# Kernel tuning notes

Hardware: AMD Instinct MI355X
Metric: run time of the kernel (lower is better)

The kernel has to match this reference:

```python
import jax, jax.numpy as jnp
import numpy as np

B, T, C, H = 2, 2048, 2048, 16
HD = C // H  # 128


def setup_inputs() -> dict:
    key = jax.random.key(0)
    k1, k2, k3 = jax.random.split(key, 3)
    x = jax.random.normal(k1, (B, T, C), jnp.float32)
    qkv_w = jax.random.normal(k2, (3 * C, C), jnp.float32) / np.float32(np.sqrt(C))
    proj_w = jax.random.normal(k3, (C, C), jnp.float32) / np.float32(np.sqrt(C))
    past = jnp.zeros((B, H, 2, T, HD), jnp.float32)  # KV cache: [B,H,2,max_seq,hd]
    return {"x": x, "qkv_w": qkv_w, "proj_w": proj_w, "past": past, "past_len": 0}


def reference(x, qkv_w, proj_w, past, past_len):
    Bx, Tx, Cx = x.shape
    hd = Cx // H
    # qkv projection (no bias), then split heads: [B,T,3C] -> [B,T,3,H,hd] -> [B,H,T,hd] each
    qkv = jnp.einsum('btc,dc->btd', x, qkv_w).reshape(Bx, Tx, 3, H, hd)
    q = jnp.transpose(qkv[:, :, 0], (0, 2, 1, 3))
    k = jnp.transpose(qkv[:, :, 1], (0, 2, 1, 3))
    v = jnp.transpose(qkv[:, :, 2], (0, 2, 1, 3))
    # KV-cache write (functional scatter) then read back the valid prefix
    past = past.at[:, :, 0, past_len:past_len + Tx].set(k)
    past = past.at[:, :, 1, past_len:past_len + Tx].set(v)
    k = past[:, :, 0, :past_len + Tx]
    v = past[:, :, 1, :past_len + Tx]
    S = past_len + Tx
    scale = np.float32(1.0 / np.sqrt(hd))
    scores = jnp.einsum('bhqd,bhkd->bhqk', q, k) * scale  # [B,H,T,S]
    if Tx > 1:  # is_causal=T>1 in the torch module (past_len=0 on this path)
        mask = jnp.arange(S)[None, :] <= (jnp.arange(Tx)[:, None] + past_len)
        scores = jnp.where(mask, scores, jnp.float32(-jnp.inf))
    attn = jax.nn.softmax(scores, axis=-1)
    out = jnp.einsum('bhqk,bhkd->bhqd', attn, v)  # [B,H,T,hd]
    out = jnp.transpose(out, (0, 2, 1, 3)).reshape(Bx, Tx, Cx)
    return jnp.einsum('btc,dc->btd', out, proj_w)
```

## Files before the change

kernel.cpp:

```cpp
#include <hip/hip_runtime.h>

typedef __bf16 bf16x8 __attribute__((ext_vector_type(8)));
typedef float f32x4 __attribute__((ext_vector_type(4)));
typedef unsigned short u16x8 __attribute__((ext_vector_type(8)));

__device__ __forceinline__ unsigned short f2bf(float f) {
  return __builtin_bit_cast(unsigned short, (__bf16)f);
}

__device__ __forceinline__ void gload16(const void* g, void* l) {
  __builtin_amdgcn_global_load_lds((const __attribute__((address_space(1))) unsigned int*)g,
                                   (__attribute__((address_space(3))) unsigned int*)l,
                                   16, 0, 0);
}

template <int N>
__device__ __forceinline__ float rormax(float x) {
  int r = __builtin_amdgcn_update_dpp(0, __builtin_bit_cast(int, x), 0x120 + N, 0xF, 0xF, true);
  return fmaxf(x, __builtin_bit_cast(float, r));
}
template <int N>
__device__ __forceinline__ float rorsum(float x) {
  int r = __builtin_amdgcn_update_dpp(0, __builtin_bit_cast(int, x), 0x120 + N, 0xF, 0xF, true);
  return x + __builtin_bit_cast(float, r);
}
__device__ __forceinline__ float red16max(float x) {
  x = rormax<8>(x); x = rormax<4>(x); x = rormax<2>(x); return rormax<1>(x);
}
__device__ __forceinline__ float red16sum(float x) {
  x = rorsum<8>(x); x = rorsum<4>(x); x = rorsum<2>(x); return rorsum<1>(x);
}

__global__ __launch_bounds__(256)
void cvt3_f32_bf16(const float* __restrict__ s0, unsigned short* __restrict__ d0, int n0,
                   const float* __restrict__ s1, unsigned short* __restrict__ d1, int n1,
                   const float* __restrict__ s2, unsigned short* __restrict__ d2)
{
  int blk = blockIdx.x;
  const float* s; unsigned short* d;
  if (blk < n0)            { s = s0; d = d0; }
  else if (blk < n0 + n1)  { s = s1; d = d1; blk -= n0; }
  else                     { s = s2; d = d2; blk -= n0 + n1; }
  const size_t e = ((size_t)blk * 256 + threadIdx.x) * 8;
  const float4 a = *(const float4*)(s + e);
  const float4 b = *(const float4*)(s + e + 4);
  u16x8 v;
  v[0] = f2bf(a.x); v[1] = f2bf(a.y); v[2] = f2bf(a.z); v[3] = f2bf(a.w);
  v[4] = f2bf(b.x); v[5] = f2bf(b.y); v[6] = f2bf(b.z); v[7] = f2bf(b.w);
  *(u16x8*)(d + e) = v;
}

#define STG(XS, Xg, buf, half, kt)                                              \
  { gload16((Xg) + (size_t)((half)*128 + srow8) * K + (kt)*64 + scol,           \
            (XS) + (buf)*32768 + (half)*16384 + wid*1024);                      \
    gload16((Xg) + (size_t)((half)*128 + 64 + srow8) * K + (kt)*64 + scol,      \
            (XS) + (buf)*32768 + (half)*16384 + 8192 + wid*1024); }

#define LDA(buf, ih)                                                            \
  { _Pragma("unroll") for (int i = 0; i < 4; ++i) {                             \
      const int ro = (buf)*32768 + arow + ((ih)*64 + i*16)*128;                 \
      af[i][0] = *(const bf16x8*)(As + ro + cbs0);                              \
      af[i][1] = *(const bf16x8*)(As + ro + cbs1); } }

#define LDB(buf, jh, BF)                                                        \
  { _Pragma("unroll") for (int j = 0; j < 2; ++j) {                             \
      const int ro = (buf)*32768 + brow + (((jh)*2 + j)*16)*128;                \
      BF[j][0] = *(const bf16x8*)(Bs + ro + cbs0);                              \
      BF[j][1] = *(const bf16x8*)(Bs + ro + cbs1); } }

#define MM(ih, jh, BF)                                                          \
  { _Pragma("unroll") for (int i = 0; i < 4; ++i)                               \
    _Pragma("unroll") for (int j = 0; j < 2; ++j)                               \
    _Pragma("unroll") for (int kk = 0; kk < 2; ++kk)                            \
      acc[(ih)*4+i][(jh)*2+j] = __builtin_amdgcn_mfma_f32_16x16x32_bf16(        \
          af[i][kk], BF[j][kk], acc[(ih)*4+i][(jh)*2+j], 0, 0, 0); }

#define BAR1_12() { asm volatile("s_waitcnt lgkmcnt(8)" ::: "memory");          \
                    __builtin_amdgcn_s_barrier();                               \
                    asm volatile("s_waitcnt lgkmcnt(0)" ::: "memory");          \
                    __builtin_amdgcn_sched_barrier(0);                          \
                    __builtin_amdgcn_s_setprio(1); }
#define BAR1()    { __builtin_amdgcn_s_barrier();                               \
                    asm volatile("s_waitcnt lgkmcnt(0)" ::: "memory");          \
                    __builtin_amdgcn_sched_barrier(0);                          \
                    __builtin_amdgcn_s_setprio(1); }
#define BAR2()    { __builtin_amdgcn_s_setprio(0); __builtin_amdgcn_s_barrier(); }
#define BAR2V()   { __builtin_amdgcn_s_setprio(0);                              \
                    asm volatile("s_waitcnt vmcnt(4)" ::: "memory");            \
                    __builtin_amdgcn_s_barrier(); }

template <bool OUTBF16>
__global__ __launch_bounds__(512, 1)
void gemm256_bt(const unsigned short* __restrict__ Ap, const unsigned short* __restrict__ Bp,
                void* __restrict__ Outp, int M, int N, int K)
{
  extern __shared__ __align__(16) char smem[];
  char* const As = smem;
  char* const Bs = smem + 65536;
  const int tid = threadIdx.x;
  const int wid = tid >> 6, lane = tid & 63;
  const int wm = wid >> 2, wn = wid & 3;
  const int lg = lane >> 4, lr = lane & 15;

  const int gx = gridDim.x;
  const int nwg = gx * (int)gridDim.y;
  int bid = (int)blockIdx.y * gx + (int)blockIdx.x;
  bid = (bid & 7) * (nwg >> 3) + (bid >> 3);
  const int m0 = (bid / gx) * 256, n0 = (bid % gx) * 256;

  const int srow8 = wid * 8 + (lane >> 3);
  const int scol  = (((lane & 7) ^ (lane >> 3)) << 3);
  const unsigned short* const Ag = Ap + (size_t)m0 * K;
  const unsigned short* const Bg = Bp + (size_t)n0 * K;

  const int cbs0 = (lg * 16) ^ ((lr & 7) << 4);
  const int cbs1 = (64 + lg * 16) ^ ((lr & 7) << 4);
  const int arow = (wm * 128 + lr) * 128;
  const int brow = (wn * 64 + lr) * 128;

  const f32x4 z4 = {0.f, 0.f, 0.f, 0.f};
  f32x4 acc[8][4];
#pragma unroll
  for (int i = 0; i < 8; ++i)
#pragma unroll
    for (int j = 0; j < 4; ++j) acc[i][j] = z4;

  const int NKT = K >> 6;
  bf16x8 af[4][2], bf01[2][2], bf23[2][2];

  STG(As, Ag, 0, 0, 0); STG(As, Ag, 0, 1, 0);
  STG(Bs, Bg, 0, 0, 0); STG(Bs, Bg, 0, 1, 0);
  STG(Bs, Bg, 1, 0, 1); STG(Bs, Bg, 1, 1, 1);
  asm volatile("s_waitcnt vmcnt(4)" ::: "memory");
  __builtin_amdgcn_s_barrier();

  for (int it = 0; it < (NKT >> 1); ++it) {
    const int t1  = 2 * it + 1;
    const int t0n = (2 * it + 2 < NKT) ? 2 * it + 2 : NKT - 1;
    const int t1n = (t1 + 2 < NKT) ? t1 + 2 : NKT - 1;

    LDA(0, 0); LDB(0, 0, bf01); STG(As, Ag, 1, 0, t1);
    BAR1_12(); MM(0, 0, bf01); BAR2();
    LDB(0, 1, bf23); STG(As, Ag, 1, 1, t1);
    BAR1(); MM(0, 1, bf23); BAR2();
    LDA(0, 1); STG(Bs, Bg, 0, 0, t0n);
    BAR1(); MM(1, 0, bf01); BAR2();
    STG(Bs, Bg, 0, 1, t0n);
    BAR1(); MM(1, 1, bf23); BAR2V();
    LDA(1, 0); LDB(1, 0, bf01); STG(As, Ag, 0, 0, t0n);
    BAR1_12(); MM(0, 0, bf01); BAR2();
    LDB(1, 1, bf23); STG(As, Ag, 0, 1, t0n);
    BAR1(); MM(0, 1, bf23); BAR2();
    LDA(1, 1); STG(Bs, Bg, 1, 0, t1n);
    BAR1(); MM(1, 0, bf01); BAR2();
    STG(Bs, Bg, 1, 1, t1n);
    BAR1(); MM(1, 1, bf23); BAR2V();
  }
  asm volatile("s_waitcnt vmcnt(0)" ::: "memory");

#pragma unroll
  for (int i = 0; i < 8; ++i)
#pragma unroll
    for (int j = 0; j < 4; ++j)
#pragma unroll
      for (int r = 0; r < 4; ++r) {
        const int row = m0 + wm * 128 + i * 16 + lg * 4 + r;
        const int col = n0 + wn * 64 + j * 16 + lr;
        const float val = acc[i][j][r];
        if (OUTBF16) ((unsigned short*)Outp)[(size_t)row * N + col] = f2bf(val);
        else         ((float*)Outp)[(size_t)row * N + col] = val;
      }
}

template <bool OUTBF16>
__global__ __launch_bounds__(256, 2)
void gemm_bt16(const unsigned short* __restrict__ Ap, const unsigned short* __restrict__ Bp,
               void* __restrict__ Outp, int M, int N, int K)
{
  __shared__ __align__(16) char smA[128 * 128];
  __shared__ __align__(16) char smB[128 * 128];
  const int tid = threadIdx.x;
  const int wid = tid >> 6, lane = tid & 63;
  const int wr = wid >> 1, wc = wid & 1;
  const int lg = lane >> 4, lr = lane & 15;

  const int gx = gridDim.x;
  const int nwg = gx * gridDim.y;
  int bid = blockIdx.y * gx + blockIdx.x;
  bid = (bid & 7) * (nwg >> 3) + (bid >> 3);
  const int m0 = (bid / gx) * 128, n0 = (bid % gx) * 128;

  const int srow = wid * 8 + (lane >> 3);
  const int scol = (((lane & 7) ^ (lane >> 3)) << 3);
  const int lbase = wid * 1024;

  const f32x4 z4 = {0.f, 0.f, 0.f, 0.f};
  f32x4 acc[4][4];
#pragma unroll
  for (int i = 0; i < 4; ++i)
#pragma unroll
    for (int j = 0; j < 4; ++j) acc[i][j] = z4;

  for (int k0 = 0; k0 < K; k0 += 64) {
    __syncthreads();
#pragma unroll
    for (int c = 0; c < 4; ++c) {
      const int row = c * 32 + srow;
      gload16(Ap + (size_t)(m0 + row) * K + k0 + scol, smA + c * 4096 + lbase);
      gload16(Bp + (size_t)(n0 + row) * K + k0 + scol, smB + c * 4096 + lbase);
    }
    __syncthreads();
#pragma unroll
    for (int kk = 0; kk < 2; ++kk) {
      const int cb = (kk * 32 + lg * 8) * 2;
      bf16x8 a4[4], b4[4];
#pragma unroll
      for (int i = 0; i < 4; ++i) {
        const int row = wr * 64 + i * 16 + lr;
        a4[i] = *(const bf16x8*)(smA + row * 128 + (cb ^ ((row & 7) << 4)));
      }
#pragma unroll
      for (int j = 0; j < 4; ++j) {
        const int row = wc * 64 + j * 16 + lr;
        b4[j] = *(const bf16x8*)(smB + row * 128 + (cb ^ ((row & 7) << 4)));
      }
#pragma unroll
      for (int i = 0; i < 4; ++i)
#pragma unroll
        for (int j = 0; j < 4; ++j)
          acc[i][j] = __builtin_amdgcn_mfma_f32_16x16x32_bf16(a4[i], b4[j], acc[i][j], 0, 0, 0);
    }
  }
#pragma unroll
  for (int i = 0; i < 4; ++i)
#pragma unroll
    for (int j = 0; j < 4; ++j)
#pragma unroll
      for (int r = 0; r < 4; ++r) {
        const int row = m0 + wr * 64 + i * 16 + lg * 4 + r;
        const int col = n0 + wc * 64 + j * 16 + lr;
        const float val = acc[i][j][r];
        if (OUTBF16) ((unsigned short*)Outp)[(size_t)row * N + col] = f2bf(val);
        else         ((float*)Outp)[(size_t)row * N + col] = val;
      }
}

__global__ __launch_bounds__(256)
void vtrans(const unsigned short* __restrict__ qkv, unsigned short* __restrict__ vT)
{
  constexpr int T = 2048, ROWS = 6144;
  const int bh = blockIdx.y, b = bh >> 4, h = bh & 15;
  const int t0 = blockIdx.x * 64;
  const int tid = threadIdx.x;
  __shared__ __align__(16) char Sc[64 * 256];

#pragma unroll
  for (int c = 0; c < 4; ++c) {
    const int row = c * 16 + (tid >> 4);
    const int col = (tid & 15) * 8;
    u16x8 v = *(const u16x8*)(qkv + (size_t)(b * T + t0 + row) * ROWS + 4096 + h * 128 + col);
    *(u16x8*)(Sc + row * 256 + ((col * 2) ^ ((row & 7) << 4))) = v;
  }
  __syncthreads();
#pragma unroll
  for (int c = 0; c < 4; ++c) {
    const int d = c * 32 + (tid >> 3);
    const int t = (tid & 7) * 8;
    u16x8 v;
#pragma unroll
    for (int i = 0; i < 8; ++i)
      v[i] = *(const unsigned short*)(Sc + (t + i) * 256 + ((d * 2) ^ (((t + i) & 7) << 4)));
    *(u16x8*)(vT + ((size_t)bh * 128 + d) * 2048 + t0 + t) = v;
  }
}

__global__ __launch_bounds__(256, 2)
void attn_fwd(const unsigned short* __restrict__ qkv, const unsigned short* __restrict__ vT,
              unsigned short* __restrict__ outp)
{
  constexpr int T = 2048, ROWS = 6144;
  const int blk = blockIdx.x;
  const int qt = 31 - (blk >> 5);
  const int bh = blk & 31;
  const int b = bh >> 4, h = bh & 15;
  const int q0 = qt * 64;
  const int tid = threadIdx.x;
  const int wid = tid >> 6, lane = tid & 63;
  const int lg = lane >> 4, lr = lane & 15;

  __shared__ __align__(16) char Ks[128 * 256];
  __shared__ __align__(16) char Vt[128 * 256];
  __shared__ __align__(16) char Ps[64 * 256];

  const int srow = wid * 4 + (lane >> 4);
  const int scol = (((lane & 15) ^ (srow & 7)) << 3);

  const size_t qrow = (size_t)(b * T + q0 + wid * 16 + lr) * ROWS + h * 128;
  bf16x8 qf[4];
#pragma unroll
  for (int kd = 0; kd < 4; ++kd)
    qf[kd] = __builtin_bit_cast(bf16x8, *(const u16x8*)(qkv + qrow + kd * 32 + lg * 8));

  const f32x4 z4 = {0.f, 0.f, 0.f, 0.f};
  f32x4 oacc[8];
#pragma unroll
  for (int jj = 0; jj < 8; ++jj) oacc[jj] = z4;
  float mrow[4] = {-1e30f, -1e30f, -1e30f, -1e30f};
  float lsum[4] = {0.f, 0.f, 0.f, 0.f};
  const float scale2 = 0.12751745f;

  const int nt = (qt >> 1) + 1;
  for (int kt = 0; kt < nt; ++kt) {
    __syncthreads();
#pragma unroll
    for (int c = 0; c < 8; ++c) {
      gload16(qkv + (size_t)(b * T + kt * 128 + c * 16 + srow) * ROWS + 2048 + h * 128 + scol,
              Ks + c * 4096 + wid * 1024);
      gload16(vT + ((size_t)bh * 128 + c * 16 + srow) * 2048 + kt * 128 + scol,
              Vt + c * 4096 + wid * 1024);
    }
    asm volatile("s_waitcnt vmcnt(0)" ::: "memory");
    __syncthreads();

    f32x4 sf[8];
#pragma unroll
    for (int j = 0; j < 8; ++j) sf[j] = z4;
#pragma unroll
    for (int kd = 0; kd < 4; ++kd) {
      const int cb = (kd * 32 + lg * 8) * 2;
#pragma unroll
      for (int j = 0; j < 8; ++j) {
        const int row = j * 16 + lr;
        bf16x8 kf = *(const bf16x8*)(Ks + row * 256 + (cb ^ ((row & 7) << 4)));
        sf[j] = __builtin_amdgcn_mfma_f32_16x16x32_bf16(qf[kd], kf, sf[j], 0, 0, 0);
      }
    }

    const bool diag = (kt == nt - 1);
#pragma unroll
    for (int j = 0; j < 8; ++j)
#pragma unroll
      for (int r = 0; r < 4; ++r) {
        float s = sf[j][r] * scale2;
        const int key = kt * 128 + j * 16 + lr;
        const int qi  = q0 + wid * 16 + lg * 4 + r;
        if (diag && key > qi) s = -1e30f;
        sf[j][r] = s;
      }
    float pm[4];
#pragma unroll
    for (int r = 0; r < 4; ++r) {
      float m0 = fmaxf(fmaxf(sf[0][r], sf[1][r]), fmaxf(sf[2][r], sf[3][r]));
      float m1 = fmaxf(fmaxf(sf[4][r], sf[5][r]), fmaxf(sf[6][r], sf[7][r]));
      pm[r] = red16max(fmaxf(m0, m1));
    }
    const float growth = fmaxf(fmaxf(pm[0] - mrow[0], pm[1] - mrow[1]),
                               fmaxf(pm[2] - mrow[2], pm[3] - mrow[3]));
    const bool resc = !__all(growth <= 11.5f);
    float alpha[4];
    if (resc) {
#pragma unroll
      for (int r = 0; r < 4; ++r) {
        const float mn = fmaxf(mrow[r], pm[r]);
        alpha[r] = exp2f(mrow[r] - mn);
        mrow[r] = mn;
      }
    }
    float rs[4] = {0.f, 0.f, 0.f, 0.f};
#pragma unroll
    for (int j = 0; j < 8; ++j)
#pragma unroll
      for (int r = 0; r < 4; ++r) {
        const float p = exp2f(sf[j][r] - mrow[r]);
        sf[j][r] = p;
        rs[r] += p;
      }
    if (resc) {
#pragma unroll
      for (int r = 0; r < 4; ++r) lsum[r] = lsum[r] * alpha[r] + red16sum(rs[r]);
    } else {
#pragma unroll
      for (int r = 0; r < 4; ++r) lsum[r] += red16sum(rs[r]);
    }

#pragma unroll
    for (int j = 0; j < 8; ++j)
#pragma unroll
      for (int r = 0; r < 4; ++r) {
        const int prow = wid * 16 + lg * 4 + r;
        const int pcol = j * 16 + lr;
        *(unsigned short*)(Ps + prow * 256 + ((pcol * 2) ^ ((prow & 7) << 4))) = f2bf(sf[j][r]);
      }
    if (resc) {
#pragma unroll
      for (int jj = 0; jj < 8; ++jj)
#pragma unroll
        for (int r = 0; r < 4; ++r) oacc[jj][r] *= alpha[r];
    }
    asm volatile("s_waitcnt lgkmcnt(0)" ::: "memory");
    __builtin_amdgcn_sched_barrier(0);

#pragma unroll
    for (int kk = 0; kk < 4; ++kk) {
      const int prow = wid * 16 + lr;
      const int pcb = (kk * 32 + lg * 8) * 2;
      bf16x8 pf = *(const bf16x8*)(Ps + prow * 256 + (pcb ^ ((prow & 7) << 4)));
#pragma unroll
      for (int jj = 0; jj < 8; ++jj) {
        const int vrow = jj * 16 + lr;
        bf16x8 vf = *(const bf16x8*)(Vt + vrow * 256 + (pcb ^ ((vrow & 7) << 4)));
        oacc[jj] = __builtin_amdgcn_mfma_f32_16x16x32_bf16(pf, vf, oacc[jj], 0, 0, 0);
      }
    }
  }

#pragma unroll
  for (int jj = 0; jj < 8; ++jj)
#pragma unroll
    for (int r = 0; r < 4; ++r) {
      const int q = q0 + wid * 16 + lg * 4 + r;
      const int col = h * 128 + jj * 16 + lr;
      const float o = oacc[jj][r] / lsum[r];
      outp[(size_t)(b * T + q) * 2048 + col] = f2bf(o);
    }
}

extern "C" void kernel_launch(void* const* d_in, const int* in_sizes, int n_in,
                              void* d_out, int out_size, void* d_ws, size_t ws_size,
                              hipStream_t stream) {
  (void)in_sizes; (void)n_in; (void)out_size; (void)ws_size;
  const float* x     = (const float*)d_in[0];
  const float* qkvw  = (const float*)d_in[1];
  const float* projw = (const float*)d_in[2];

  unsigned short* qkvb   = (unsigned short*)d_ws;
  unsigned short* attnb  = qkvb   + (size_t)4096 * 6144;
  unsigned short* xb     = attnb  + (size_t)4096 * 2048;
  unsigned short* qkvwb  = xb     + (size_t)4096 * 2048;
  unsigned short* projwb = qkvwb  + (size_t)6144 * 2048;
  unsigned short* vT     = xb;
  float* out = (float*)d_out;

  static bool attr_set = false;
  if (!attr_set) {
    hipFuncSetAttribute((const void*)gemm256_bt<true>,
                        hipFuncAttributeMaxDynamicSharedMemorySize, 131072);
    attr_set = true;
  }

  cvt3_f32_bf16<<<4096 + 6144 + 2048, 256, 0, stream>>>(
      x, xb, 4096, qkvw, qkvwb, 6144, projw, projwb);
  gemm256_bt<true><<<dim3(6144 / 256, 4096 / 256), 512, 131072, stream>>>(
      xb, qkvwb, qkvb, 4096, 6144, 2048);
  vtrans<<<dim3(32, 32), 256, 0, stream>>>(qkvb, vT);
  attn_fwd<<<1024, 256, 0, stream>>>(qkvb, vT, attnb);
  gemm_bt16<false><<<dim3(2048 / 128, 4096 / 128), 256, 0, stream>>>(
      attnb, projwb, out, 4096, 2048, 2048);
}
```

Before: 256.0 us.

## Process 128 query rows per attention block to halve K/V tile loads

Each attention block now handles two 64-row query sub-blocks (128 queries) against every loaded K/V tile, so each K/V tile is loaded into shared memory half as often. The P matrix is written into the K tile buffer after an extra barrier, which drops the separate P buffer. The grid shrinks from 1024 to 512 blocks and uses a zig-zag tile order to balance the causal work. Register pressure doubles for the accumulators and scores, which may cut occupancy, and the smaller grid leaves fewer blocks for load balancing on the GPU.

```diff
diff --git a/kernel.cpp b/kernel.cpp
--- a/kernel.cpp
+++ b/kernel.cpp
@@ -280,36 +280,44 @@
 {
   constexpr int T = 2048, ROWS = 6144;
   const int blk = blockIdx.x;
-  const int qt = 31 - (blk >> 5);
+  const int g = blk >> 5;
+  const int qt = (g < 8) ? 15 - g : g - 8;
   const int bh = blk & 31;
   const int b = bh >> 4, h = bh & 15;
-  const int q0 = qt * 64;
+  const int q0 = qt * 128;
   const int tid = threadIdx.x;
   const int wid = tid >> 6, lane = tid & 63;
   const int lg = lane >> 4, lr = lane & 15;
 
   __shared__ __align__(16) char Ks[128 * 256];
   __shared__ __align__(16) char Vt[128 * 256];
-  __shared__ __align__(16) char Ps[64 * 256];
 
   const int srow = wid * 4 + (lane >> 4);
   const int scol = (((lane & 15) ^ (srow & 7)) << 3);
 
-  const size_t qrow = (size_t)(b * T + q0 + wid * 16 + lr) * ROWS + h * 128;
-  bf16x8 qf[4];
-#pragma unroll
-  for (int kd = 0; kd < 4; ++kd)
-    qf[kd] = __builtin_bit_cast(bf16x8, *(const u16x8*)(qkv + qrow + kd * 32 + lg * 8));
+  bf16x8 qf[2][4];
+#pragma unroll
+  for (int rb = 0; rb < 2; ++rb) {
+    const size_t qrow = (size_t)(b * T + q0 + rb * 64 + wid * 16 + lr) * ROWS + h * 128;
+#pragma unroll
+    for (int kd = 0; kd < 4; ++kd)
+      qf[rb][kd] = __builtin_bit_cast(bf16x8, *(const u16x8*)(qkv + qrow + kd * 32 + lg * 8));
+  }
 
   const f32x4 z4 = {0.f, 0.f, 0.f, 0.f};
-  f32x4 oacc[8];
-#pragma unroll
-  for (int jj = 0; jj < 8; ++jj) oacc[jj] = z4;
-  float mrow[4] = {-1e30f, -1e30f, -1e30f, -1e30f};
-  float lsum[4] = {0.f, 0.f, 0.f, 0.f};
+  f32x4 oacc[2][8];
+#pragma unroll
+  for (int rb = 0; rb < 2; ++rb)
+#pragma unroll
+    for (int jj = 0; jj < 8; ++jj) oacc[rb][jj] = z4;
+  float mrow[2][4], lsum[2][4];
+#pragma unroll
+  for (int rb = 0; rb < 2; ++rb)
+#pragma unroll
+    for (int r = 0; r < 4; ++r) { mrow[rb][r] = -1e30f; lsum[rb][r] = 0.f; }
   const float scale2 = 0.12751745f;
 
-  const int nt = (qt >> 1) + 1;
+  const int nt = qt + 1;
   for (int kt = 0; kt < nt; ++kt) {
     __syncthreads();
 #pragma unroll
@@ -322,9 +330,11 @@
     asm volatile("s_waitcnt vmcnt(0)" ::: "memory");
     __syncthreads();
 
-    f32x4 sf[8];
-#pragma unroll
-    for (int j = 0; j < 8; ++j) sf[j] = z4;
+    f32x4 sf[2][8];
+#pragma unroll
+    for (int rb = 0; rb < 2; ++rb)
+#pragma unroll
+      for (int j = 0; j < 8; ++j) sf[rb][j] = z4;
 #pragma unroll
     for (int kd = 0; kd < 4; ++kd) {
       const int cb = (kd * 32 + lg * 8) * 2;
@@ -332,97 +342,122 @@
       for (int j = 0; j < 8; ++j) {
         const int row = j * 16 + lr;
         bf16x8 kf = *(const bf16x8*)(Ks + row * 256 + (cb ^ ((row & 7) << 4)));
-        sf[j] = __builtin_amdgcn_mfma_f32_16x16x32_bf16(qf[kd], kf, sf[j], 0, 0, 0);
+        sf[0][j] = __builtin_amdgcn_mfma_f32_16x16x32_bf16(qf[0][kd], kf, sf[0][j], 0, 0, 0);
+        sf[1][j] = __builtin_amdgcn_mfma_f32_16x16x32_bf16(qf[1][kd], kf, sf[1][j], 0, 0, 0);
       }
     }
 
     const bool diag = (kt == nt - 1);
-#pragma unroll
-    for (int j = 0; j < 8; ++j)
+    float pm[2][4];
+#pragma unroll
+    for (int rb = 0; rb < 2; ++rb) {
+#pragma unroll
+      for (int j = 0; j < 8; ++j)
+#pragma unroll
+        for (int r = 0; r < 4; ++r) {
+          float s = sf[rb][j][r] * scale2;
+          const int key = kt * 128 + j * 16 + lr;
+          const int qi  = q0 + rb * 64 + wid * 16 + lg * 4 + r;
+          if (diag && key > qi) s = -1e30f;
+          sf[rb][j][r] = s;
+        }
 #pragma unroll
       for (int r = 0; r < 4; ++r) {
-        float s = sf[j][r] * scale2;
-        const int key = kt * 128 + j * 16 + lr;
-        const int qi  = q0 + wid * 16 + lg * 4 + r;
-        if (diag && key > qi) s = -1e30f;
-        sf[j][r] = s;
-      }
-    float pm[4];
-#pragma unroll
-    for (int r = 0; r < 4; ++r) {
-      float m0 = fmaxf(fmaxf(sf[0][r], sf[1][r]), fmaxf(sf[2][r], sf[3][r]));
-      float m1 = fmaxf(fmaxf(sf[4][r], sf[5][r]), fmaxf(sf[6][r], sf[7][r]));
-      pm[r] = red16max(fmaxf(m0, m1));
-    }
-    const float growth = fmaxf(fmaxf(pm[0] - mrow[0], pm[1] - mrow[1]),
-                               fmaxf(pm[2] - mrow[2], pm[3] - mrow[3]));
+        float a0 = fmaxf(fmaxf(sf[rb][0][r], sf[rb][1][r]), fmaxf(sf[rb][2][r], sf[rb][3][r]));
+        float a1 = fmaxf(fmaxf(sf[rb][4][r], sf[rb][5][r]), fmaxf(sf[rb][6][r], sf[rb][7][r]));
+        pm[rb][r] = red16max(fmaxf(a0, a1));
+      }
+    }
+    float growth = -1e30f;
+#pragma unroll
+    for (int rb = 0; rb < 2; ++rb)
+#pragma unroll
+      for (int r = 0; r < 4; ++r) growth = fmaxf(growth, pm[rb][r] - mrow[rb][r]);
     const bool resc = !__all(growth <= 11.5f);
-    float alpha[4];
+    float alpha[2][4];
     if (resc) {
 #pragma unroll
-      for (int r = 0; r < 4; ++r) {
-        const float mn = fmaxf(mrow[r], pm[r]);
-        alpha[r] = exp2f(mrow[r] - mn);
-        mrow[r] = mn;
-      }
-    }
-    float rs[4] = {0.f, 0.f, 0.f, 0.f};
-#pragma unroll
-    for (int j = 0; j < 8; ++j)
-#pragma unroll
-      for (int r = 0; r < 4; ++r) {
-        const float p = exp2f(sf[j][r] - mrow[r]);
-        sf[j][r] = p;
-        rs[r] += p;
-      }
+      for (int rb = 0; rb < 2; ++rb)
+#pragma unroll
+        for (int r = 0; r < 4; ++r) {
+          const float mn = fmaxf(mrow[rb][r], pm[rb][r]);
+          alpha[rb][r] = exp2f(mrow[rb][r] - mn);
+          mrow[rb][r] = mn;
+        }
+    }
+    float rs[2][4] = {{0.f, 0.f, 0.f, 0.f}, {0.f, 0.f, 0.f, 0.f}};
+#pragma unroll
+    for (int rb = 0; rb < 2; ++rb)
+#pragma unroll
+      for (int j = 0; j < 8; ++j)
+#pragma unroll
+        for (int r = 0; r < 4; ++r) {
+          const float p = exp2f(sf[rb][j][r] - mrow[rb][r]);
+          sf[rb][j][r] = p;
+          rs[rb][r] += p;
+        }
+#pragma unroll
+    for (int rb = 0; rb < 2; ++rb) {
+      if (resc) {
+#pragma unroll
+        for (int r = 0; r < 4; ++r) lsum[rb][r] = lsum[rb][r] * alpha[rb][r] + red16sum(rs[rb][r]);
+      } else {
+#pragma unroll
+        for (int r = 0; r < 4; ++r) lsum[rb][r] += red16sum(rs[rb][r]);
+      }
+    }
+
+    __syncthreads();
+
+#pragma unroll
+    for (int rb = 0; rb < 2; ++rb)
+#pragma unroll
+      for (int j = 0; j < 8; ++j)
+#pragma unroll
+        for (int r = 0; r < 4; ++r) {
+          const int prow = rb * 64 + wid * 16 + lg * 4 + r;
+          const int pcol = j * 16 + lr;
+          *(unsigned short*)(Ks + prow * 256 + ((pcol * 2) ^ ((prow & 7) << 4))) = f2bf(sf[rb][j][r]);
+        }
     if (resc) {
 #pragma unroll
-      for (int r = 0; r < 4; ++r) lsum[r] = lsum[r] * alpha[r] + red16sum(rs[r]);
-    } else {
-#pragma unroll
-      for (int r = 0; r < 4; ++r) lsum[r] += red16sum(rs[r]);
-    }
-
-#pragma unroll
-    for (int j = 0; j < 8; ++j)
-#pragma unroll
-      for (int r = 0; r < 4; ++r) {
-        const int prow = wid * 16 + lg * 4 + r;
-        const int pcol = j * 16 + lr;
-        *(unsigned short*)(Ps + prow * 256 + ((pcol * 2) ^ ((prow & 7) << 4))) = f2bf(sf[j][r]);
-      }
-    if (resc) {
-#pragma unroll
-      for (int jj = 0; jj < 8; ++jj)
-#pragma unroll
-        for (int r = 0; r < 4; ++r) oacc[jj][r] *= alpha[r];
+      for (int rb = 0; rb < 2; ++rb)
+#pragma unroll
+        for (int jj = 0; jj < 8; ++jj)
+#pragma unroll
+          for (int r = 0; r < 4; ++r) oacc[rb][jj][r] *= alpha[rb][r];
     }
     asm volatile("s_waitcnt lgkmcnt(0)" ::: "memory");
     __builtin_amdgcn_sched_barrier(0);
 
 #pragma unroll
     for (int kk = 0; kk < 4; ++kk) {
-      const int prow = wid * 16 + lr;
       const int pcb = (kk * 32 + lg * 8) * 2;
-      bf16x8 pf = *(const bf16x8*)(Ps + prow * 256 + (pcb ^ ((prow & 7) << 4)));
+      const int prow0 = wid * 16 + lr;
+      const int prow1 = 64 + wid * 16 + lr;
+      bf16x8 pf0 = *(const bf16x8*)(Ks + prow0 * 256 + (pcb ^ ((prow0 & 7) << 4)));
+      bf16x8 pf1 = *(const bf16x8*)(Ks + prow1 * 256 + (pcb ^ ((prow1 & 7) << 4)));
 #pragma unroll
       for (int jj = 0; jj < 8; ++jj) {
         const int vrow = jj * 16 + lr;
         bf16x8 vf = *(const bf16x8*)(Vt + vrow * 256 + (pcb ^ ((vrow & 7) << 4)));
-        oacc[jj] = __builtin_amdgcn_mfma_f32_16x16x32_bf16(pf, vf, oacc[jj], 0, 0, 0);
-      }
-    }
-  }
-
-#pragma unroll
-  for (int jj = 0; jj < 8; ++jj)
-#pragma unroll
-    for (int r = 0; r < 4; ++r) {
-      const int q = q0 + wid * 16 + lg * 4 + r;
-      const int col = h * 128 + jj * 16 + lr;
-      const float o = oacc[jj][r] / lsum[r];
-      outp[(size_t)(b * T + q) * 2048 + col] = f2bf(o);
-    }
+        oacc[0][jj] = __builtin_amdgcn_mfma_f32_16x16x32_bf16(pf0, vf, oacc[0][jj], 0, 0, 0);
+        oacc[1][jj] = __builtin_amdgcn_mfma_f32_16x16x32_bf16(pf1, vf, oacc[1][jj], 0, 0, 0);
+      }
+    }
+  }
+
+#pragma unroll
+  for (int rb = 0; rb < 2; ++rb)
+#pragma unroll
+    for (int jj = 0; jj < 8; ++jj)
+#pragma unroll
+      for (int r = 0; r < 4; ++r) {
+        const int q = q0 + rb * 64 + wid * 16 + lg * 4 + r;
+        const int col = h * 128 + jj * 16 + lr;
+        const float o = oacc[rb][jj][r] / lsum[rb][r];
+        outp[(size_t)(b * T + q) * 2048 + col] = f2bf(o);
+      }
 }
 
 extern "C" void kernel_launch(void* const* d_in, const int* in_sizes, int n_in,
@@ -453,7 +488,7 @@
   gemm256_bt<true><<<dim3(6144 / 256, 4096 / 256), 512, 131072, stream>>>(
       xb, qkvwb, qkvb, 4096, 6144, 2048);
   vtrans<<<dim3(32, 32), 256, 0, stream>>>(qkvb, vT);
-  attn_fwd<<<1024, 256, 0, stream>>>(qkvb, vT, attnb);
+  attn_fwd<<<512, 256, 0, stream>>>(qkvb, vT, attnb);
   gemm_bt16<false><<<dim3(2048 / 128, 4096 / 128), 256, 0, stream>>>(
       attnb, projwb, out, 4096, 2048, 2048);
 }
```

Result: slower. 356.9 us (+39.4%).
